# Kernel tuning notes

Measured on AMD Instinct MI355X. Metric: run time of the kernel, lower is better.

Reference implementation:

```python
import jax, jax.numpy as jnp
import numpy as np
from jax import lax

B, T, K = 4096, 512, 2048  # students, timesteps, skills


def setup_inputs() -> dict:
    key = jax.random.key(0)
    k1, k2, k3 = jax.random.split(key, 3)
    skills = jax.random.randint(k1, (B, T), 0, K, dtype=jnp.int32)
    responses = (jax.random.uniform(k2, (B, T)) < 0.7).astype(jnp.float32)
    kp = jax.random.split(k3, 4)
    k0 = jax.random.uniform(kp[0], (K,), minval=0.05, maxval=0.85)  # initial mastery per skill
    t = jax.random.uniform(kp[1], (K,), minval=0.01, maxval=0.30)   # transit
    g = jax.random.uniform(kp[2], (K,), minval=0.05, maxval=0.30)   # guess
    s = jax.random.uniform(kp[3], (K,), minval=0.01, maxval=0.10)   # slip
    return {"skills": skills, "responses": responses, "k0": k0, "t": t, "g": g, "s": s, "num_skills": K}


def _bkt_forward(skills, responses, k0, t, g, s, num_skills):
    # Batched BKT inter_predict: per-student per-skill mastery recurrence.
    Bb, Tt = skills.shape
    rows = jnp.arange(Bb)

    def step(carry, xs):
        last, seen = carry              # [B, K] mastery state, [B, K] seen mask
        sk, res = xs                    # [B] skill ids, [B] responses at this timestep
        lm = last[rows, sk]             # gather current per-skill mastery
        sn = seen[rows, sk]
        kk = k0[sk]; tt = t[sk]; gg = g[sk]; ss = s[sk]
        # first time a skill is seen -> prior k0, else last posterior
        pL = jnp.where(sn, lm, kk)
        # Bayesian posterior given observed response
        p_corr = pL * (1.0 - ss) / (pL * (1.0 - ss) + (1.0 - pL) * gg)
        p_inc = pL * ss / (pL * ss + (1.0 - pL) * (1.0 - gg))
        p = jnp.where(res == 1.0, p_corr, p_inc)
        nxt = p + (1.0 - p) * tt        # learning transition
        last = last.at[rows, sk].set(nxt)
        seen = seen.at[rows, sk].set(True)
        return (last, seen), pL          # emitted mastery BEFORE update (as in original)

    init = (jnp.zeros((Bb, num_skills), responses.dtype),
            jnp.zeros((Bb, num_skills), dtype=bool))
    _, mastery = lax.scan(step, init, (skills.T, responses.T))  # [T, B]
    return mastery.T  # [B, T]


def reference(skills, responses, k0, t, g, s, num_skills):
    return _bkt_forward(skills, responses, k0, t, g, s, num_skills)
```

## Files before the change

kernel.cpp:

```cpp
#include <hip/hip_runtime.h>
#include <limits.h>


#define BKT_B 4096
#define BKT_T 512
#define BKT_K 2048
#define BLK   256
#define TPT   (BKT_T / BLK)
#define PTR_END 0x3FF

__device__ __forceinline__ float bkt_update(float p, int rbit, float ss,
                                            float gg, float tt) {
  float num, den;
  if (rbit) {
    num = p * (1.0f - ss);
    den = num + (1.0f - p) * gg;
  } else {
    num = p * ss;
    den = num + (1.0f - p) * (1.0f - gg);
  }
  const float q = num / den;
  return q + (1.0f - q) * tt;
}

__global__ __launch_bounds__(BLK, 8) void bkt_kernel(
    const int* __restrict__ skills,
    const float* __restrict__ resp,
    const float* __restrict__ k0,
    const float* __restrict__ tp,
    const float* __restrict__ gp,
    const float* __restrict__ sp,
    float* __restrict__ out) {
  __shared__ int head_s[BKT_K];
  __shared__ int node_s[BKT_T];

  const int b = blockIdx.x;
  const int base = b * BKT_T;
  const int tid = threadIdx.x;

  int   sk[TPT];
  float rr[TPT];
#pragma unroll
  for (int u = 0; u < TPT; ++u) {
    const int t = tid + u * BLK;
    sk[u] = skills[base + t];
    rr[u] = resp[base + t];
  }
  float k0v[TPT], ssv[TPT], ggv[TPT], ttv[TPT];
#pragma unroll
  for (int u = 0; u < TPT; ++u) {
    k0v[u] = k0[sk[u]];
    ssv[u] = sp[sk[u]];
    ggv[u] = gp[sk[u]];
    ttv[u] = tp[sk[u]];
  }

  {
    int4* h4 = (int4*)head_s;
#pragma unroll
    for (int i = 0; i < 2; ++i)
      h4[tid + i * BLK] = make_int4(-1, -1, -1, -1);
  }
  __syncthreads();

#pragma unroll
  for (int u = 0; u < TPT; ++u) {
    const int t = tid + u * BLK;
    const int old = atomicExch(&head_s[sk[u]], t);
    const int ptr = (old < 0) ? PTR_END : old;
    node_s[t] = ptr | ((rr[u] > 0.5f ? 1 : 0) << 10);
  }
  __syncthreads();

#pragma unroll
  for (int u = 0; u < TPT; ++u) {
    const int t = tid + u * BLK;
    const int head = head_s[sk[u]];

    int rank = 0, minj = INT_MAX, minnode = 0;
    for (int j = head; j >= 0; ) {
      const int node = node_s[j];
      if (j < t) {
        ++rank;
        if (j < minj) { minj = j; minnode = node; }
      }
      const int nx = node & PTR_END;
      j = (nx == PTR_END) ? -1 : nx;
    }

    float p = k0v[u];

    if (rank > 0) {
      const float ss = ssv[u];
      const float gg = ggv[u];
      const float tt = ttv[u];
      p = bkt_update(p, (minnode >> 10) & 1, ss, gg, tt);
      int cur = minj;
      for (int rd = 1; rd < rank; ++rd) {
        int best = INT_MAX, bestnode = 0;
        for (int j = head; j >= 0; ) {
          const int node = node_s[j];
          if (j < t && j > cur && j < best) { best = j; bestnode = node; }
          const int nx = node & PTR_END;
          j = (nx == PTR_END) ? -1 : nx;
        }
        p = bkt_update(p, (bestnode >> 10) & 1, ss, gg, tt);
        cur = best;
      }
    }

    out[base + t] = p;
  }
}

extern "C" void kernel_launch(void* const* d_in, const int* in_sizes, int n_in,
                              void* d_out, int out_size, void* d_ws, size_t ws_size,
                              hipStream_t stream) {
  const int*   skills = (const int*)d_in[0];
  const float* resp   = (const float*)d_in[1];
  const float* k0     = (const float*)d_in[2];
  const float* tp     = (const float*)d_in[3];
  const float* gp     = (const float*)d_in[4];
  const float* sp     = (const float*)d_in[5];
  float* out = (float*)d_out;

  bkt_kernel<<<BKT_B, BLK, 0, stream>>>(skills, resp, k0, tp, gp, sp, out);
}
```

Baseline: 17.37 us.

## Process two students per block with interleaved list walks and two-minimum tracking

Each block now handles two students, and each thread owns four timesteps loaded as int2/float2 vectors. The four linked-list traversals per thread are interleaved in one loop to expose memory-level parallelism on LDS reads. The first pass records the two smallest predecessors, so the rescans are skipped whenever a skill occurs at most twice before. In exchange it doubles shared memory per block and raises register pressure, which may reduce occupancy, and the param loads for s/g/t are deferred into the compute phase.

```diff
diff --git a/kernel.cpp b/kernel.cpp
--- a/kernel.cpp
+++ b/kernel.cpp
@@ -6,7 +6,8 @@
 #define BKT_T 512
 #define BKT_K 2048
 #define BLK   256
-#define TPT   (BKT_T / BLK)
+#define NST   2
+#define NCH   (2 * NST)
 #define PTR_END 0x3FF
 
 __device__ __forceinline__ float bkt_update(float p, int rbit, float ss,
@@ -31,85 +32,108 @@
     const float* __restrict__ gp,
     const float* __restrict__ sp,
     float* __restrict__ out) {
-  __shared__ int head_s[BKT_K];
-  __shared__ int node_s[BKT_T];
+  __shared__ int head_s[NST][BKT_K];
+  __shared__ int node_s[NST][BKT_T];
 
-  const int b = blockIdx.x;
-  const int base = b * BKT_T;
+  const int blk = blockIdx.x;
   const int tid = threadIdx.x;
 
-  int   sk[TPT];
-  float rr[TPT];
+  int skr[NCH], rbit[NCH];
 #pragma unroll
-  for (int u = 0; u < TPT; ++u) {
-    const int t = tid + u * BLK;
-    sk[u] = skills[base + t];
-    rr[u] = resp[base + t];
-  }
-  float k0v[TPT], ssv[TPT], ggv[TPT], ttv[TPT];
-#pragma unroll
-  for (int u = 0; u < TPT; ++u) {
-    k0v[u] = k0[sk[u]];
-    ssv[u] = sp[sk[u]];
-    ggv[u] = gp[sk[u]];
-    ttv[u] = tp[sk[u]];
+  for (int s = 0; s < NST; ++s) {
+    const int base = (blk * NST + s) * BKT_T;
+    const int2   skv = ((const int2*)(skills + base))[tid];
+    const float2 rrv = ((const float2*)(resp + base))[tid];
+    skr[2 * s]     = skv.x;
+    skr[2 * s + 1] = skv.y;
+    rbit[2 * s]     = rrv.x > 0.5f ? 1 : 0;
+    rbit[2 * s + 1] = rrv.y > 0.5f ? 1 : 0;
   }
 
   {
-    int4* h4 = (int4*)head_s;
+    int4* h4 = (int4*)&head_s[0][0];
 #pragma unroll
-    for (int i = 0; i < 2; ++i)
+    for (int i = 0; i < NST * BKT_K / 4 / BLK; ++i)
       h4[tid + i * BLK] = make_int4(-1, -1, -1, -1);
   }
   __syncthreads();
 
 #pragma unroll
-  for (int u = 0; u < TPT; ++u) {
-    const int t = tid + u * BLK;
-    const int old = atomicExch(&head_s[sk[u]], t);
-    const int ptr = (old < 0) ? PTR_END : old;
-    node_s[t] = ptr | ((rr[u] > 0.5f ? 1 : 0) << 10);
+  for (int c = 0; c < NCH; ++c) {
+    const int s = c >> 1;
+    const int t = 2 * tid + (c & 1);
+    const int old = atomicExch(&head_s[s][skr[c]], t);
+    node_s[s][t] = ((old < 0) ? PTR_END : old) | (rbit[c] << 10);
   }
   __syncthreads();
 
+  float k0v[NCH];
 #pragma unroll
-  for (int u = 0; u < TPT; ++u) {
-    const int t = tid + u * BLK;
-    const int head = head_s[sk[u]];
+  for (int c = 0; c < NCH; ++c)
+    k0v[c] = k0[skr[c]];
 
-    int rank = 0, minj = INT_MAX, minnode = 0;
-    for (int j = head; j >= 0; ) {
-      const int node = node_s[j];
-      if (j < t) {
-        ++rank;
-        if (j < minj) { minj = j; minnode = node; }
-      }
-      const int nx = node & PTR_END;
-      j = (nx == PTR_END) ? -1 : nx;
-    }
-
-    float p = k0v[u];
-
-    if (rank > 0) {
-      const float ss = ssv[u];
-      const float gg = ggv[u];
-      const float tt = ttv[u];
-      p = bkt_update(p, (minnode >> 10) & 1, ss, gg, tt);
-      int cur = minj;
-      for (int rd = 1; rd < rank; ++rd) {
-        int best = INT_MAX, bestnode = 0;
-        for (int j = head; j >= 0; ) {
-          const int node = node_s[j];
-          if (j < t && j > cur && j < best) { best = j; bestnode = node; }
-          const int nx = node & PTR_END;
-          j = (nx == PTR_END) ? -1 : nx;
+  int headv[NCH], j[NCH], rank[NCH], mn1[NCH], mn2[NCH], nd1[NCH], nd2[NCH];
+#pragma unroll
+  for (int c = 0; c < NCH; ++c) {
+    headv[c] = head_s[c >> 1][skr[c]];
+    j[c] = headv[c];
+    rank[c] = 0;
+    mn1[c] = INT_MAX; mn2[c] = INT_MAX; nd1[c] = 0; nd2[c] = 0;
+  }
+  while (j[0] >= 0 || j[1] >= 0 || j[2] >= 0 || j[3] >= 0) {
+#pragma unroll
+    for (int c = 0; c < NCH; ++c) {
+      if (j[c] >= 0) {
+        const int nd = node_s[c >> 1][j[c]];
+        const int t = 2 * tid + (c & 1);
+        if (j[c] < t) {
+          ++rank[c];
+          if (j[c] < mn1[c]) {
+            mn2[c] = mn1[c]; nd2[c] = nd1[c]; mn1[c] = j[c]; nd1[c] = nd;
+          } else if (j[c] < mn2[c]) {
+            mn2[c] = j[c]; nd2[c] = nd;
+          }
         }
-        p = bkt_update(p, (bestnode >> 10) & 1, ss, gg, tt);
-        cur = best;
+        const int nx = nd & PTR_END;
+        j[c] = (nx == PTR_END) ? -1 : nx;
       }
     }
+  }
 
-    out[base + t] = p;
+  float pv[NCH];
+#pragma unroll
+  for (int c = 0; c < NCH; ++c) {
+    float p = k0v[c];
+    if (rank[c] > 0) {
+      const int s_ = skr[c];
+      const int t = 2 * tid + (c & 1);
+      const float ss = sp[s_];
+      const float gg = gp[s_];
+      const float tt = tp[s_];
+      p = bkt_update(p, (nd1[c] >> 10) & 1, ss, gg, tt);
+      if (rank[c] > 1) {
+        p = bkt_update(p, (nd2[c] >> 10) & 1, ss, gg, tt);
+        int cur = mn2[c];
+        for (int rd = 2; rd < rank[c]; ++rd) {
+          int best = INT_MAX, bestnode = 0;
+          for (int jj = headv[c]; jj >= 0; ) {
+            const int nd = node_s[c >> 1][jj];
+            if (jj < t && jj > cur && jj < best) { best = jj; bestnode = nd; }
+            const int nx = nd & PTR_END;
+            jj = (nx == PTR_END) ? -1 : nx;
+          }
+          p = bkt_update(p, (bestnode >> 10) & 1, ss, gg, tt);
+          cur = best;
+        }
+      }
+    }
+    pv[c] = p;
+  }
+
+#pragma unroll
+  for (int s = 0; s < NST; ++s) {
+    const int base = (blk * NST + s) * BKT_T;
+    ((float2*)(out + base))[tid] = make_float2(pv[2 * s], pv[2 * s + 1]);
   }
 }
 
@@ -124,5 +148,5 @@
   const float* sp     = (const float*)d_in[5];
   float* out = (float*)d_out;
 
-  bkt_kernel<<<BKT_B, BLK, 0, stream>>>(skills, resp, k0, tp, gp, sp, out);
+  bkt_kernel<<<BKT_B / NST, BLK, 0, stream>>>(skills, resp, k0, tp, gp, sp, out);
 }
```

Measured after the change: 15.29 us. 11.9% less time.
